# Performance work log

Hardware: AMD Instinct MI355X
Metric: run time of the kernel (lower is better)

The kernel has to match this reference:

```python
import jax, jax.numpy as jnp
import numpy as np

N, D = 8192, 256


def setup_inputs() -> dict:
    key = jax.random.key(0)
    ka, kb = jax.random.split(key)
    latent_a = jax.random.normal(ka, (N, D), dtype=jnp.float32)
    latent_b = jax.random.normal(kb, (N, D), dtype=jnp.float32)
    return {"latent_a": latent_a, "latent_b": latent_b}


def _rbf_kernel(x, y):
    # kernel[i,j] = exp(-mean_d((x_i - y_j)^2) / D) = exp(-||x_i - y_j||^2 / D^2)
    d = x.shape[1]
    sq = (
        jnp.sum(x * x, axis=1)[:, None]
        + jnp.sum(y * y, axis=1)[None, :]
        - 2.0 * (x @ y.T)
    )  # [Nx, Ny] squared distances (no O(N^2 D) intermediate)
    return jnp.exp(-sq / (d * d))


def reference(latent_a, latent_b):
    x = latent_a.reshape(latent_a.shape[0], -1)
    y = latent_b.reshape(latent_b.shape[0], -1)
    x_kernel = _rbf_kernel(x, x)
    y_kernel = _rbf_kernel(y, y)
    xy_kernel = _rbf_kernel(x, y)
    return jnp.mean(x_kernel) + jnp.mean(y_kernel) - 2.0 * jnp.mean(xy_kernel)
```

## Files before the change

kernel.cpp:

```cpp
#include <hip/hip_runtime.h>
#include <math.h>


#define NPTS  8192
#define DIM   256
#define MTOT  (2 * NPTS)
#define TILE  128
#define BK    64
#define NTILE (MTOT / TILE)
#define XTILE (NPTS / TILE)
#define NTRI  (NTILE * (NTILE + 1) / 2)

typedef int   i32x4 __attribute__((ext_vector_type(4)));
typedef float f32x4 __attribute__((ext_vector_type(4)));

#define SQF   21.0f
#define NSCF  (-2.20135502845565e-5f)
#define C2S   (9.983580e-8f)

#define GLDS(g, l)                                                          \
    __builtin_amdgcn_global_load_lds(                                       \
        (const __attribute__((address_space(1))) void*)(g),                 \
        (__attribute__((address_space(3))) void*)(l), 16, 0, 0)

__global__ __launch_bounds__(256) void mmd_prep(const float* __restrict__ a,
                                                const float* __restrict__ b,
                                                char* __restrict__ z8,
                                                float* __restrict__ nsc) {
    const int row  = blockIdx.x * 4 + (threadIdx.x >> 6);
    const int lane = threadIdx.x & 63;
    const float* src = (row < NPTS) ? (a + (size_t)row * DIM)
                                    : (b + (size_t)(row - NPTS) * DIM);
    float4 v = *reinterpret_cast<const float4*>(src + lane * 4);
    float s = v.x * v.x + v.y * v.y + v.z * v.z + v.w * v.w;

    int q0 = __float2int_rn(fminf(fmaxf(v.x * SQF, -127.f), 127.f));
    int q1 = __float2int_rn(fminf(fmaxf(v.y * SQF, -127.f), 127.f));
    int q2 = __float2int_rn(fminf(fmaxf(v.z * SQF, -127.f), 127.f));
    int q3 = __float2int_rn(fminf(fmaxf(v.w * SQF, -127.f), 127.f));
    uint packed = (q0 & 0xFF) | ((q1 & 0xFF) << 8) |
                  ((q2 & 0xFF) << 16) | ((uint)(q3 & 0xFF) << 24);
    *reinterpret_cast<uint*>(&z8[(size_t)row * DIM + lane * 4]) = packed;

    #pragma unroll
    for (int off = 32; off > 0; off >>= 1) s += __shfl_down(s, off);
    if (lane == 0) nsc[row] = s * NSCF;
}

__device__ __forceinline__ void unrank(int p, int& I, int& J) {
    I = (int)(NTILE + 0.5 - sqrt((NTILE + 0.5) * (NTILE + 0.5) - 2.0 * p));
    int base = I * NTILE - I * (I - 1) / 2;
    if (p < base)                     { --I; base = I * NTILE - I * (I - 1) / 2; }
    else if (p >= base + (NTILE - I)) { ++I; base = I * NTILE - I * (I - 1) / 2; }
    J = I + (p - base);
}

__global__ __launch_bounds__(256, 4) void mmd_gram(const char* __restrict__ z8,
                                                   const float* __restrict__ nsc,
                                                   double* __restrict__ partials) {
    int I, J;
    unrank(blockIdx.x, I, J);

    __shared__ char sI[TILE * BK];
    __shared__ char sJ[TILE * BK];
    __shared__ double wsum[4];

    const int t   = threadIdx.x;
    const int l   = t & 63;
    const int wid = t >> 6;
    const int wy  = (wid >> 1) * 64;
    const int wx  = (wid & 1) * 64;

    const int   rbase = (wid & 1) * 64;
    const char* gtile = z8 + (size_t)(((wid < 2) ? I : J) * TILE) * DIM;
    char*       ltile = (wid < 2) ? sI : sJ;
    const int   rloc = l >> 2;
    const int   gch  = (l & 3) ^ (l >> 4);
    const char* gsrc = gtile + (size_t)(rbase + rloc) * DIM + gch * 16;
    char*       ldst = ltile + rbase * BK + l * 16;

    i32x4 acc[4][4];
    #pragma unroll
    for (int bi = 0; bi < 4; ++bi)
        #pragma unroll
        for (int bj = 0; bj < 4; ++bj)
            acc[bi][bj] = (i32x4)0;

    const int ar = l & 15;
    const int ch = ((l >> 4) ^ (ar >> 2)) * 16;

    for (int k0 = 0; k0 < DIM; k0 += BK) {
        __syncthreads();
        #pragma unroll
        for (int g = 0; g < 4; ++g)
            GLDS(gsrc + (size_t)g * 16 * DIM + k0, ldst + g * 16 * BK);
        __syncthreads();

        i32x4 aF[4];
        #pragma unroll
        for (int bi = 0; bi < 4; ++bi)
            aF[bi] = *reinterpret_cast<const i32x4*>(&sI[(wy + bi * 16 + ar) * BK + ch]);
        #pragma unroll
        for (int bj = 0; bj < 4; ++bj) {
            i32x4 bF = *reinterpret_cast<const i32x4*>(&sJ[(wx + bj * 16 + ar) * BK + ch]);
            #pragma unroll
            for (int bi = 0; bi < 4; ++bi)
                acc[bi][bj] = __builtin_amdgcn_mfma_i32_16x16x64_i8(
                                  aF[bi], bF, acc[bi][bj], 0, 0, 0);
        }
    }

    const int rg = (l >> 4) * 4;
    float racc0 = 0.f, racc1 = 0.f, racc2 = 0.f, racc3 = 0.f;
    #pragma unroll
    for (int bi = 0; bi < 4; ++bi) {
        float ni[4];
        #pragma unroll
        for (int r = 0; r < 4; ++r)
            ni[r] = nsc[I * TILE + wy + bi * 16 + rg + r];
        float rs = 0.f;
        #pragma unroll
        for (int bj = 0; bj < 4; ++bj) {
            const float nj = nsc[J * TILE + wx + bj * 16 + (l & 15)];
            #pragma unroll
            for (int r = 0; r < 4; ++r)
                rs += exp2f(fmaf((float)acc[bi][bj][r], C2S, ni[r] + nj));
        }
        if (bi == 0) racc0 = rs; else if (bi == 1) racc1 = rs;
        else if (bi == 2) racc2 = rs; else racc3 = rs;
    }

    double tsum = ((double)racc0 + racc1) + ((double)racc2 + racc3);
    const double sgn  = ((I < XTILE) == (J < XTILE)) ? 1.0 : -1.0;
    const double mult = (I == J) ? sgn : 2.0 * sgn;
    tsum *= mult;

    #pragma unroll
    for (int off = 32; off > 0; off >>= 1) tsum += __shfl_down(tsum, off);
    if (l == 0) wsum[wid] = tsum;
    __syncthreads();
    if (t == 0) partials[blockIdx.x] = wsum[0] + wsum[1] + wsum[2] + wsum[3];
}

__global__ __launch_bounds__(256) void mmd_reduce(const double* __restrict__ partials,
                                                  float* __restrict__ out) {
    double s = 0.0;
    for (int i = threadIdx.x; i < NTRI; i += 256) s += partials[i];
    #pragma unroll
    for (int off = 32; off > 0; off >>= 1) s += __shfl_down(s, off);
    __shared__ double wsum[4];
    const int wid = threadIdx.x >> 6, lane = threadIdx.x & 63;
    if (lane == 0) wsum[wid] = s;
    __syncthreads();
    if (threadIdx.x == 0)
        out[0] = (float)((wsum[0] + wsum[1] + wsum[2] + wsum[3]) /
                         ((double)NPTS * (double)NPTS));
}

extern "C" void kernel_launch(void* const* d_in, const int* in_sizes, int n_in,
                              void* d_out, int out_size, void* d_ws, size_t ws_size,
                              hipStream_t stream) {
    const float* a = (const float*)d_in[0];
    const float* b = (const float*)d_in[1];
    float* out = (float*)d_out;

    char*   z8    = (char*)d_ws;
    float*  nsc   = (float*)(z8 + (size_t)MTOT * DIM);
    double* partials = (double*)(nsc + MTOT);

    mmd_prep<<<MTOT / 4, 256, 0, stream>>>(a, b, z8, nsc);
    mmd_gram<<<NTRI, 256, 0, stream>>>(z8, nsc, partials);
    mmd_reduce<<<1, 256, 0, stream>>>(partials, out);
}
```

Measured before the change: 137.9 us.

## Double-buffer LDS tiles to overlap global loads with MFMA compute

Replaces the single-buffered K loop, which synchronised twice per step, with two LDS buffers and a fully unrolled four-step schedule. Each step issues the async global-to-LDS loads for the next K slice before computing on the current one. It also stages the per-row norm scales for both tiles into shared memory, so the epilogue reads them from LDS instead of global memory. LDS use doubles, which may reduce how many blocks fit on each CU.

New measurement: 142.5 us. +3.3%, slower.

```diff
diff --git a/kernel.cpp b/kernel.cpp
--- a/kernel.cpp
+++ b/kernel.cpp
@@ -11,8 +11,7 @@
 #define XTILE (NPTS / TILE)
 #define NTRI  (NTILE * (NTILE + 1) / 2)
 
-typedef int   i32x4 __attribute__((ext_vector_type(4)));
-typedef float f32x4 __attribute__((ext_vector_type(4)));
+typedef int i32x4 __attribute__((ext_vector_type(4)));
 
 #define SQF   21.0f
 #define NSCF  (-2.20135502845565e-5f)
@@ -61,8 +60,9 @@
     int I, J;
     unrank(blockIdx.x, I, J);
 
-    __shared__ char sI[TILE * BK];
-    __shared__ char sJ[TILE * BK];
+    __shared__ __attribute__((aligned(16))) char sI0[TILE * BK], sJ0[TILE * BK];
+    __shared__ __attribute__((aligned(16))) char sI1[TILE * BK], sJ1[TILE * BK];
+    __shared__ float  snI[TILE], snJ[TILE];
     __shared__ double wsum[4];
 
     const int t   = threadIdx.x;
@@ -71,13 +71,25 @@
     const int wy  = (wid >> 1) * 64;
     const int wx  = (wid & 1) * 64;
 
+    if (t < TILE) snI[t] = nsc[I * TILE + t];
+    else          snJ[t - TILE] = nsc[J * TILE + (t - TILE)];
+
     const int   rbase = (wid & 1) * 64;
     const char* gtile = z8 + (size_t)(((wid < 2) ? I : J) * TILE) * DIM;
-    char*       ltile = (wid < 2) ? sI : sJ;
+    const bool  isI   = (wid < 2);
     const int   rloc = l >> 2;
     const int   gch  = (l & 3) ^ (l >> 4);
-    const char* gsrc = gtile + (size_t)(rbase + rloc) * DIM + gch * 16;
-    char*       ldst = ltile + rbase * BK + l * 16;
+    const char* gsrc  = gtile + (size_t)(rbase + rloc) * DIM + gch * 16;
+    const int   ldoff = rbase * BK + l * 16;
+
+#define STAGE(dI, dJ, k0)                                                   \
+    do {                                                                    \
+        char* ld = (isI ? (dI) : (dJ)) + ldoff;                             \
+        const char* gs = gsrc + (k0);                                       \
+        _Pragma("unroll")                                                   \
+        for (int g = 0; g < 4; ++g)                                         \
+            GLDS(gs + (size_t)g * 16 * DIM, ld + g * 16 * BK);              \
+    } while (0)
 
     i32x4 acc[4][4];
     #pragma unroll
@@ -89,26 +101,30 @@
     const int ar = l & 15;
     const int ch = ((l >> 4) ^ (ar >> 2)) * 16;
 
-    for (int k0 = 0; k0 < DIM; k0 += BK) {
-        __syncthreads();
-        #pragma unroll
-        for (int g = 0; g < 4; ++g)
-            GLDS(gsrc + (size_t)g * 16 * DIM + k0, ldst + g * 16 * BK);
-        __syncthreads();
+#define COMPUTE(cI, cJ)                                                     \
+    do {                                                                    \
+        i32x4 aF[4];                                                        \
+        _Pragma("unroll")                                                   \
+        for (int bi = 0; bi < 4; ++bi)                                      \
+            aF[bi] = *reinterpret_cast<const i32x4*>(                       \
+                         &(cI)[(wy + bi * 16 + ar) * BK + ch]);             \
+        _Pragma("unroll")                                                   \
+        for (int bj = 0; bj < 4; ++bj) {                                    \
+            i32x4 bF = *reinterpret_cast<const i32x4*>(                     \
+                         &(cJ)[(wx + bj * 16 + ar) * BK + ch]);             \
+            _Pragma("unroll")                                               \
+            for (int bi = 0; bi < 4; ++bi)                                  \
+                acc[bi][bj] = __builtin_amdgcn_mfma_i32_16x16x64_i8(        \
+                                  aF[bi], bF, acc[bi][bj], 0, 0, 0);        \
+        }                                                                   \
+    } while (0)
 
-        i32x4 aF[4];
-        #pragma unroll
-        for (int bi = 0; bi < 4; ++bi)
-            aF[bi] = *reinterpret_cast<const i32x4*>(&sI[(wy + bi * 16 + ar) * BK + ch]);
-        #pragma unroll
-        for (int bj = 0; bj < 4; ++bj) {
-            i32x4 bF = *reinterpret_cast<const i32x4*>(&sJ[(wx + bj * 16 + ar) * BK + ch]);
-            #pragma unroll
-            for (int bi = 0; bi < 4; ++bi)
-                acc[bi][bj] = __builtin_amdgcn_mfma_i32_16x16x64_i8(
-                                  aF[bi], bF, acc[bi][bj], 0, 0, 0);
-        }
-    }
+    STAGE(sI0, sJ0, 0);
+    __syncthreads();
+    STAGE(sI1, sJ1, BK);     COMPUTE(sI0, sJ0);  __syncthreads();
+    STAGE(sI0, sJ0, 2 * BK); COMPUTE(sI1, sJ1);  __syncthreads();
+    STAGE(sI1, sJ1, 3 * BK); COMPUTE(sI0, sJ0);  __syncthreads();
+    COMPUTE(sI1, sJ1);
 
     const int rg = (l >> 4) * 4;
     float racc0 = 0.f, racc1 = 0.f, racc2 = 0.f, racc3 = 0.f;
@@ -117,11 +133,11 @@
         float ni[4];
         #pragma unroll
         for (int r = 0; r < 4; ++r)
-            ni[r] = nsc[I * TILE + wy + bi * 16 + rg + r];
+            ni[r] = snI[wy + bi * 16 + rg + r];
         float rs = 0.f;
         #pragma unroll
         for (int bj = 0; bj < 4; ++bj) {
-            const float nj = nsc[J * TILE + wx + bj * 16 + (l & 15)];
+            const float nj = snJ[wx + bj * 16 + (l & 15)];
             #pragma unroll
             for (int r = 0; r < 4; ++r)
                 rs += exp2f(fmaf((float)acc[bi][bj][r], C2S, ni[r] + nj));
```
